# Kernel tuning notes

Measured on AMD Instinct MI355X. Metric: run time of the kernel, lower is better.

## Reference

```python
import jax, jax.numpy as jnp
import numpy as np

DIM = 256; HEADS = 8; DK = 64; DV = 64; FH = 32; FW = 32; B = 16
INK = HEADS * DK; INV = HEADS * DV; N = FH * FW
SCALE = DK ** -0.5; EPS = 1e-5


def _pos_indices():
    pos = np.stack(np.meshgrid(np.arange(FH), np.arange(FW), indexing='ij'), axis=-1).reshape(-1, 2)
    rel = np.abs(pos[:, None, :] - pos[None, :, :])  # [N,N,2]
    return jnp.asarray(rel[..., 0] * FW + rel[..., 1], jnp.int32)  # [N,N]


def _bn(x, g, b, m, v):
    # eval-mode BatchNorm2d over channel axis 1
    s = (g / jnp.sqrt(v + EPS))
    return x * s[None, :, None, None] + (b - m * s)[None, :, None, None]


def setup_inputs() -> dict:
    key = jax.random.key(0)
    ks = jax.random.split(key, 24)
    f32 = jnp.float32
    def bn_params(k, c):
        k1, k2, k3, k4 = jax.random.split(k, 4)
        return (jax.random.normal(k1, (c,), f32) * 0.1 + 1.0,
                jax.random.normal(k2, (c,), f32) * 0.1,
                jax.random.normal(k3, (c,), f32) * 0.1,
                jax.random.uniform(k4, (c,), f32) + 0.5)
    gq, bq, mq, vq = bn_params(ks[1], INK)
    gk, bk, mk, vk = bn_params(ks[3], INK)
    gv, bv, mv, vv = bn_params(ks[5], INV)
    go, bo, mo, vo = bn_params(ks[7], DIM)
    return {
        'x': jax.random.normal(ks[0], (B, DIM, FH, FW), f32),
        'wq': jax.random.normal(ks[2], (INK, DIM), f32) * (DIM ** -0.5),
        'gq': gq, 'bq': bq, 'mq': mq, 'vq': vq,
        'wk': jax.random.normal(ks[4], (INK, DIM), f32) * (DIM ** -0.5),
        'gk': gk, 'bk': bk, 'mk': mk, 'vk': vk,
        'wv': jax.random.normal(ks[6], (INV, DIM), f32) * (DIM ** -0.5),
        'gv': gv, 'bv': bv, 'mv': mv, 'vv': vv,
        'emb': jax.random.normal(ks[8], (N, HEADS), f32) * 0.02,
        'w_out': jax.random.normal(ks[9], (DIM, INV), f32) * (INV ** -0.5),
        'b_out': jax.random.normal(ks[10], (DIM,), f32) * 0.02,
        'go': go, 'bo': bo, 'mo': mo, 'vo': vo,
        'pos_indices': _pos_indices(),
    }


def reference(x, wq, gq, bq, mq, vq, wk, gk, bk, mk, vk, wv, gv, bv, mv, vv,
              emb, w_out, b_out, go, bo, mo, vo, pos_indices):
    b = x.shape[0]
    # 1x1 conv == channel matmul
    q = _bn(jnp.einsum('bchw,oc->bohw', x, wq), gq, bq, mq, vq)
    k = _bn(jnp.einsum('bchw,oc->bohw', x, wk), gk, bk, mk, vk)
    v = _bn(jnp.einsum('bchw,oc->bohw', x, wv), gv, bv, mv, vv)
    # 'b (h d) x y -> b h (x y) d'
    def split_heads(t, d):
        return t.reshape(b, HEADS, d, N).transpose(0, 1, 3, 2)
    q = split_heads(q, DK); k = split_heads(k, DK); v = split_heads(v, DV)
    dots = jnp.einsum('bhid,bhjd->bhij', q, k) * SCALE  # [b,h,N,N]
    bias = emb[pos_indices]                               # [N,N,h] gather
    dots = dots + jnp.transpose(bias, (2, 0, 1))[None] / SCALE
    attn = jax.nn.softmax(dots, axis=-1)
    out = jnp.einsum('bhij,bhjd->bhid', attn, v)
    out = out.transpose(0, 1, 3, 2).reshape(b, INV, FH, FW)  # 'b h (x y) d -> b (h d) x y'
    hs = out * jnp.clip(out + 3.0, 0.0, 6.0) / 6.0           # Hardswish
    y = jnp.einsum('bchw,oc->bohw', hs, w_out) + b_out[None, :, None, None]
    return _bn(y, go, bo, mo, vo)
```

## Files before the change

kernel.cpp:

```cpp
#include <hip/hip_runtime.h>

typedef __attribute__((ext_vector_type(4))) float f32x4;
typedef __attribute__((ext_vector_type(8))) _Float16 f16x8;
typedef __attribute__((ext_vector_type(4))) _Float16 f16x4;

static __device__ __forceinline__ f32x4 mfma16f(f16x8 a, f16x8 b, f32x4 c) {
    return __builtin_amdgcn_mfma_f32_16x16x32_f16(a, b, c, 0, 0, 0);
}

__global__ __launch_bounds__(256) void prep(
    const float* __restrict__ x,
    const float* __restrict__ s0, const float* __restrict__ s1,
    const float* __restrict__ s2, const float* __restrict__ s3,
    _Float16* __restrict__ d0h, _Float16* __restrict__ d0l,
    _Float16* __restrict__ d1h, _Float16* __restrict__ d1l,
    _Float16* __restrict__ d2h, _Float16* __restrict__ d2l,
    _Float16* __restrict__ d3h, _Float16* __restrict__ d3l,
    _Float16* __restrict__ xth, _Float16* __restrict__ xtl)
{
    __shared__ float lt[32][36];
    const int t = threadIdx.x;
    const int bid = blockIdx.x;
    if (bid < 2048) {
        const int seg = bid >> 9;
        const int i = (bid & 511) * 256 + t;
        const float* src = (seg == 0) ? s0 : (seg == 1) ? s1 : (seg == 2) ? s2 : s3;
        _Float16* dh = (seg == 0) ? d0h : (seg == 1) ? d1h : (seg == 2) ? d2h : d3h;
        _Float16* dl = (seg == 0) ? d0l : (seg == 1) ? d1l : (seg == 2) ? d2l : d3l;
        const float f = src[i];
        const _Float16 h = (_Float16)f;
        dh[i] = h;
        dl[i] = (_Float16)(f - (float)h);
    } else {
        const int bid2 = bid - 2048;
        const int c0 = (bid2 & 7) * 32, hw0 = ((bid2 >> 3) & 31) * 32, b = bid2 >> 8;
        {
            const int cl = t >> 3, hw4 = (t & 7) * 4;
            *(f32x4*)&lt[cl][hw4] = *(const f32x4*)&x[((size_t)(b * 256 + c0 + cl)) * 1024 + hw0 + hw4];
        }
        __syncthreads();
        {
            const int hwl = t >> 3, c4 = (t & 7) * 4;
            f16x4 hv, lv;
#pragma unroll
            for (int e = 0; e < 4; ++e) {
                const float f = lt[c4 + e][hwl];
                const _Float16 h = (_Float16)f;
                hv[e] = h;
                lv[e] = (_Float16)(f - (float)h);
            }
            const size_t off = ((size_t)(b * 1024 + hw0 + hwl)) * 256 + c0 + c4;
            *(f16x4*)(xth + off) = hv;
            *(f16x4*)(xtl + off) = lv;
        }
    }
}

__global__ __launch_bounds__(256, 4) void qkv_mfma(
    const _Float16* __restrict__ xth, const _Float16* __restrict__ xtl,
    const _Float16* __restrict__ wqh, const _Float16* __restrict__ wql,
    const _Float16* __restrict__ wkh, const _Float16* __restrict__ wkl,
    const _Float16* __restrict__ wvh, const _Float16* __restrict__ wvl,
    const float* __restrict__ gq, const float* __restrict__ bq, const float* __restrict__ mq, const float* __restrict__ vq,
    const float* __restrict__ gk, const float* __restrict__ bk, const float* __restrict__ mk, const float* __restrict__ vk,
    const float* __restrict__ gv, const float* __restrict__ bv, const float* __restrict__ mv, const float* __restrict__ vv,
    _Float16* __restrict__ qh, _Float16* __restrict__ ql,
    _Float16* __restrict__ kh,
    _Float16* __restrict__ vt)
{
    __shared__ _Float16 Ah[128][64];
    __shared__ _Float16 Al[128][64];
    __shared__ float sc_l[64], tc_l[64];

    const int t = threadIdx.x;
    const int bn = blockIdx.x;
    const int m0 = blockIdx.y * 128;
    const int proj = bn >> 3;
    const int o0 = (bn & 7) * 64;
    const int bimg = m0 >> 10;
    const int nb = m0 & 1023;

    const _Float16* Wh = (proj == 0) ? wqh : (proj == 1) ? wkh : wvh;
    const _Float16* Wl = (proj == 0) ? wql : (proj == 1) ? wkl : wvl;
    const float* G  = (proj == 0) ? gq : (proj == 1) ? gk : gv;
    const float* Bt = (proj == 0) ? bq : (proj == 1) ? bk : bv;
    const float* Mn = (proj == 0) ? mq : (proj == 1) ? mk : mv;
    const float* Vr = (proj == 0) ? vq : (proj == 1) ? vk : vv;

    if (t < 64) {
        const int o = o0 + t;
        float s = G[o] / sqrtf(Vr[o] + 1e-5f);
        float tt = Bt[o] - Mn[o] * s;
        if (proj == 0) { s *= 0.125f; tt *= 0.125f; }
        sc_l[t] = s; tc_l[t] = tt;
    }

    const int wave = t >> 6, lane = t & 63;
    const int quad = lane >> 4, l16 = lane & 15;
    const int wm = (wave >> 1) * 64;
    const int wn = (wave & 1) * 32;

    const int srow = wave * 32;
    const int lr8 = lane >> 3;
    const int lsl = lane & 7;

    f32x4 acc[8] = {};

    for (int c0 = 0; c0 < 256; c0 += 64) {
#pragma unroll
        for (int p = 0; p < 4; ++p) {
            const int r = srow + p * 8 + lr8;
            const int sg = lsl ^ (r & 7);
            const size_t goff = ((size_t)(bimg * 1024 + nb + r)) * 256 + c0 + sg * 8;
            __builtin_amdgcn_global_load_lds(
                (const __attribute__((address_space(1))) void*)(xth + goff),
                (__attribute__((address_space(3))) void*)&Ah[srow + p * 8][0], 16, 0, 0);
            __builtin_amdgcn_global_load_lds(
                (const __attribute__((address_space(1))) void*)(xtl + goff),
                (__attribute__((address_space(3))) void*)&Al[srow + p * 8][0], 16, 0, 0);
        }
        __syncthreads();

#pragma unroll
        for (int kk = 0; kk < 2; ++kk) {
            f16x8 ah[4], al[4], bh[2], bl[2];
#pragma unroll
            for (int nj = 0; nj < 2; ++nj) {
                const size_t off = ((size_t)(o0 + wn + nj * 16 + l16)) * 256 + c0 + kk * 32 + quad * 8;
                bh[nj] = *(const f16x8*)(Wh + off);
                if (proj < 2) bl[nj] = *(const f16x8*)(Wl + off);
            }
#pragma unroll
            for (int mi = 0; mi < 4; ++mi) {
                const int arow = wm + mi * 16 + l16;
                const int sl = ((kk * 4 + quad) ^ (arow & 7)) * 8;
                ah[mi] = *(const f16x8*)&Ah[arow][sl];
                al[mi] = *(const f16x8*)&Al[arow][sl];
            }
            if (proj < 2) {
#pragma unroll
                for (int nj = 0; nj < 2; ++nj)
#pragma unroll
                    for (int mi = 0; mi < 4; ++mi) {
                        f32x4 a = acc[nj * 4 + mi];
                        a = mfma16f(bh[nj], ah[mi], a);
                        a = mfma16f(bh[nj], al[mi], a);
                        a = mfma16f(bl[nj], ah[mi], a);
                        acc[nj * 4 + mi] = a;
                    }
            } else {
#pragma unroll
                for (int mi = 0; mi < 4; ++mi)
#pragma unroll
                    for (int nj = 0; nj < 2; ++nj) {
                        f32x4 a = acc[mi * 2 + nj];
                        a = mfma16f(ah[mi], bh[nj], a);
                        a = mfma16f(al[mi], bh[nj], a);
                        acc[mi * 2 + nj] = a;
                    }
            }
        }
        __syncthreads();
    }

    if (proj < 2) {
        _Float16* Oh = (proj == 0) ? qh : kh;
#pragma unroll
        for (int nj = 0; nj < 2; ++nj) {
            const int olb = wn + nj * 16 + quad * 4;
            const int ob = o0 + olb;
            const int head = ob >> 6, d0 = ob & 63;
#pragma unroll
            for (int mi = 0; mi < 4; ++mi) {
                const int n = nb + wm + mi * 16 + l16;
                f16x4 hv, lv;
#pragma unroll
                for (int rr = 0; rr < 4; ++rr) {
                    const float val = acc[nj * 4 + mi][rr] * sc_l[olb + rr] + tc_l[olb + rr];
                    const _Float16 h = (_Float16)val;
                    hv[rr] = h;
                    lv[rr] = (_Float16)(val - (float)h);
                }
                const size_t off = (((size_t)(bimg * 8 + head)) * 1024 + n) * 64 + d0;
                *(f16x4*)(Oh + off) = hv;
                if (proj == 0) *(f16x4*)(ql + off) = lv;
            }
        }
    } else {
#pragma unroll
        for (int nj = 0; nj < 2; ++nj) {
            const int olb = wn + nj * 16 + l16;
            const int o = o0 + olb;
            const int head = o >> 6, d = o & 63;
            const float s = sc_l[olb], tt = tc_l[olb];
#pragma unroll
            for (int mi = 0; mi < 4; ++mi) {
                const int n0 = nb + wm + mi * 16 + quad * 4;
                f16x4 v4;
#pragma unroll
                for (int rr = 0; rr < 4; ++rr) v4[rr] = (_Float16)(acc[mi * 2 + nj][rr] * s + tt);
                *(f16x4*)(vt + (((size_t)(bimg * 8 + head)) * 64 + d) * 1024 + n0) = v4;
            }
        }
    }
}

__global__ __launch_bounds__(512, 4) void attn_mfma(
    const _Float16* __restrict__ qh, const _Float16* __restrict__ ql,
    const _Float16* __restrict__ kh,
    const _Float16* __restrict__ vt,
    const float* __restrict__ emb,
    _Float16* __restrict__ hsh)
{
    __shared__ float    emb_s[1024];
    __shared__ _Float16 kth[64][76];
    __shared__ _Float16 vts[64][76];

    const int t = threadIdx.x;
    const int bid = blockIdx.x;
    const int bh = bid & 127, qb = bid >> 7;
    const int b = bh >> 3, h = bh & 7;
    const int wave = t >> 6, lane = t & 63;
    const int quad = lane >> 4, l16 = lane & 15;
    const int q0 = qb * 128 + wave * 16;
    const float L2E = 1.44269504f;

    for (int i = t; i < 1024; i += 512) emb_s[i] = (8.0f * emb[i * 8 + h] - 12.0f) * L2E;

    const size_t base = (size_t)bh * 65536;

    f16x8 qfh[2], qfl[2];
#pragma unroll
    for (int kk = 0; kk < 2; ++kk) {
        const size_t off = base + (size_t)(q0 + l16) * 64 + kk * 32 + quad * 8;
        qfh[kk] = *(const f16x8*)(qh + off);
        qfl[kk] = *(const f16x8*)(ql + off);
    }

    const int ig0 = q0 + l16;
    const int xi = ig0 >> 5, yi = ig0 & 31;

    const int sr = t >> 3;
    const int scs = (t & 7) * 8;

    f16x8 pkh, pvv;
    pkh = *(const f16x8*)(kh + base + (size_t)sr * 64 + scs);
    pvv = *(const f16x8*)(vt + base + (size_t)sr * 1024 + scs);

    f32x4 ao[4] = {};
    float lsum = 0.0f;

    for (int jb = 0; jb < 16; ++jb) {
        __syncthreads();
        *(f16x8*)&kth[sr][scs] = pkh;
        *(f16x8*)&vts[sr][scs] = pvv;
        __syncthreads();
        if (jb < 15) {
            pkh = *(const f16x8*)(kh + base + (size_t)((jb + 1) * 64 + sr) * 64 + scs);
            pvv = *(const f16x8*)(vt + base + (size_t)sr * 1024 + (jb + 1) * 64 + scs);
        }

#pragma unroll
        for (int nj = 0; nj < 4; ++nj) {
            const f16x8 kf0 = *(const f16x8*)&kth[nj * 16 + l16][quad * 8];
            const f16x8 kf1 = *(const f16x8*)&kth[nj * 16 + l16][32 + quad * 8];

            f32x4 ss = {};
            __builtin_amdgcn_s_setprio(1);
            ss = mfma16f(kf0, qfh[0], ss);
            ss = mfma16f(kf0, qfl[0], ss);
            ss = mfma16f(kf1, qfh[1], ss);
            ss = mfma16f(kf1, qfl[1], ss);
            __builtin_amdgcn_s_setprio(0);

            const int xj = 2 * jb + (nj >> 1);
            const int yj0 = ((nj & 1) << 4) + quad * 4;
            const int dxo = abs(xi - xj) << 5;
            const int yq = yi - yj0;
            const float p0 = __builtin_amdgcn_exp2f(fmaf(ss[0], L2E, emb_s[dxo + abs(yq)]));
            const float p1 = __builtin_amdgcn_exp2f(fmaf(ss[1], L2E, emb_s[dxo + abs(yq - 1)]));
            const float p2 = __builtin_amdgcn_exp2f(fmaf(ss[2], L2E, emb_s[dxo + abs(yq - 2)]));
            const float p3 = __builtin_amdgcn_exp2f(fmaf(ss[3], L2E, emb_s[dxo + abs(yq - 3)]));
            lsum += (p0 + p1) + (p2 + p3);
            f16x4 pa;
            pa[0] = (_Float16)p0; pa[1] = (_Float16)p1;
            pa[2] = (_Float16)p2; pa[3] = (_Float16)p3;

            f16x4 vf[4];
#pragma unroll
            for (int dj = 0; dj < 4; ++dj)
                vf[dj] = *(const f16x4*)&vts[dj * 16 + l16][nj * 16 + quad * 4];
            __builtin_amdgcn_s_setprio(1);
#pragma unroll
            for (int dj = 0; dj < 4; ++dj)
                ao[dj] = __builtin_amdgcn_mfma_f32_16x16x16f16(pa, vf[dj], ao[dj], 0, 0, 0);
            __builtin_amdgcn_s_setprio(0);
        }
    }

    float l = lsum;
    l += __shfl_xor(l, 16, 64);
    l += __shfl_xor(l, 32, 64);
    float inv[4];
#pragma unroll
    for (int r = 0; r < 4; ++r)
        inv[r] = 1.0f / __shfl(l, quad * 4 + r, 64);
#pragma unroll
    for (int r = 0; r < 4; ++r) {
        const int ig = q0 + quad * 4 + r;
#pragma unroll
        for (int dj = 0; dj < 4; ++dj) {
            const float o = ao[dj][r] * inv[r];
            const float hsw = o * fminf(fmaxf(o + 3.0f, 0.0f), 6.0f) * (1.0f / 6.0f);
            hsh[((size_t)(b * 1024 + ig)) * 512 + h * 64 + dj * 16 + l16] = (_Float16)hsw;
        }
    }
}

__global__ __launch_bounds__(256) void out_mfma(
    const _Float16* __restrict__ hsh,
    const _Float16* __restrict__ woh, const _Float16* __restrict__ wol,
    const float* __restrict__ b_out, const float* __restrict__ go, const float* __restrict__ bo,
    const float* __restrict__ mo, const float* __restrict__ vo, float* __restrict__ y)
{
    __shared__ _Float16 Ah[64][136];

    const int t = threadIdx.x;
    const int m0 = blockIdx.x * 64;
    const int o0 = blockIdx.y * 128;
    const int bimg = m0 >> 10, nb = m0 & 1023;
    const int wave = t >> 6, lane = t & 63;
    const int quad = lane >> 4, l16 = lane & 15;
    const int wm = (wave >> 1) * 32, wn = (wave & 1) * 64;

    f32x4 acc[2][4] = {};
    f16x8 bh[4], bl[4], nbh[4], nbl[4];

#pragma unroll
    for (int nj = 0; nj < 4; ++nj) {
        const size_t off = ((size_t)(o0 + wn + nj * 16 + l16)) * 512 + quad * 8;
        bh[nj] = *(const f16x8*)(woh + off);
        bl[nj] = *(const f16x8*)(wol + off);
    }

#pragma unroll
    for (int it = 0; it < 16; ++it) {
        const int c0 = (it >> 2) * 128, kk = it & 3;
        if (kk == 0) {
            __syncthreads();
            const int cs = (t & 7) * 16;
#pragma unroll
            for (int p = 0; p < 2; ++p) {
                const int r = (t >> 3) + p * 32;
                *(f16x8*)&Ah[r][cs]     = *(const f16x8*)(hsh + ((size_t)(m0 + r)) * 512 + c0 + cs);
                *(f16x8*)&Ah[r][cs + 8] = *(const f16x8*)(hsh + ((size_t)(m0 + r)) * 512 + c0 + cs + 8);
            }
            __syncthreads();
        }
        if (it < 15) {
            const int nit = it + 1;
            const int nc0 = (nit >> 2) * 128, nkk = nit & 3;
#pragma unroll
            for (int nj = 0; nj < 4; ++nj) {
                const size_t off = ((size_t)(o0 + wn + nj * 16 + l16)) * 512 + nc0 + nkk * 32 + quad * 8;
                nbh[nj] = *(const f16x8*)(woh + off);
                nbl[nj] = *(const f16x8*)(wol + off);
            }
        }
        f16x8 ah[2];
#pragma unroll
        for (int mi = 0; mi < 2; ++mi)
            ah[mi] = *(const f16x8*)&Ah[wm + mi * 16 + l16][kk * 32 + quad * 8];
#pragma unroll
        for (int mi = 0; mi < 2; ++mi)
#pragma unroll
            for (int nj = 0; nj < 4; ++nj) {
                acc[mi][nj] = mfma16f(ah[mi], bh[nj], acc[mi][nj]);
                acc[mi][nj] = mfma16f(ah[mi], bl[nj], acc[mi][nj]);
            }
#pragma unroll
        for (int nj = 0; nj < 4; ++nj) { bh[nj] = nbh[nj]; bl[nj] = nbl[nj]; }
    }

#pragma unroll
    for (int nj = 0; nj < 4; ++nj) {
        const int o = o0 + wn + nj * 16 + l16;
        const float s = go[o] / sqrtf(vo[o] + 1e-5f);
        const float tt = bo[o] - mo[o] * s;
        const float bf = b_out[o];
#pragma unroll
        for (int mi = 0; mi < 2; ++mi) {
            const int hw = nb + wm + mi * 16 + quad * 4;
            f32x4 v4;
#pragma unroll
            for (int rr = 0; rr < 4; ++rr) v4[rr] = (acc[mi][nj][rr] + bf) * s + tt;
            *(f32x4*)&y[((size_t)(bimg * 256 + o)) * 1024 + hw] = v4;
        }
    }
}

extern "C" void kernel_launch(void* const* d_in, const int* in_sizes, int n_in,
                              void* d_out, int out_size, void* d_ws, size_t ws_size,
                              hipStream_t stream) {
    const float* x     = (const float*)d_in[0];
    const float* wq    = (const float*)d_in[1];
    const float* gq    = (const float*)d_in[2];
    const float* bq    = (const float*)d_in[3];
    const float* mq    = (const float*)d_in[4];
    const float* vq    = (const float*)d_in[5];
    const float* wk    = (const float*)d_in[6];
    const float* gk    = (const float*)d_in[7];
    const float* bk    = (const float*)d_in[8];
    const float* mk    = (const float*)d_in[9];
    const float* vk    = (const float*)d_in[10];
    const float* wv    = (const float*)d_in[11];
    const float* gv    = (const float*)d_in[12];
    const float* bv    = (const float*)d_in[13];
    const float* mv    = (const float*)d_in[14];
    const float* vv    = (const float*)d_in[15];
    const float* emb   = (const float*)d_in[16];
    const float* w_out = (const float*)d_in[17];
    const float* b_out = (const float*)d_in[18];
    const float* go    = (const float*)d_in[19];
    const float* bo    = (const float*)d_in[20];
    const float* mo    = (const float*)d_in[21];
    const float* vo    = (const float*)d_in[22];

    _Float16* us = (_Float16*)d_ws;
    _Float16* xth = us;
    _Float16* xtl = us + 4194304;
    _Float16* hsh = us;
    _Float16* wsp = us + 16777216;
    _Float16* wqh = wsp,            *wql = wsp + 131072;
    _Float16* wkh = wsp + 262144,   *wkl = wsp + 393216;
    _Float16* wvh = wsp + 524288,   *wvl = wsp + 655360;
    _Float16* woh = wsp + 786432,   *wol = wsp + 917504;
    _Float16* qv  = us + 17825792;
    _Float16* qhw = qv,             *qlw = qv + 8388608;
    _Float16* khw = qv + 16777216;
    _Float16* vtw = qv + 33554432;

    prep<<<6144, 256, 0, stream>>>(x, wq, wk, wv, w_out,
                                   wqh, wql, wkh, wkl, wvh, wvl, woh, wol,
                                   xth, xtl);

    qkv_mfma<<<dim3(24, 128), 256, 0, stream>>>(
        xth, xtl, wqh, wql, wkh, wkl, wvh, wvl,
        gq, bq, mq, vq, gk, bk, mk, vk, gv, bv, mv, vv,
        qhw, qlw, khw, vtw);

    attn_mfma<<<1024, 512, 0, stream>>>(
        qhw, qlw, khw, vtw, emb, hsh);

    out_mfma<<<dim3(256, 2), 256, 0, stream>>>(
        hsh, woh, wol, b_out, go, bo, mo, vo, (float*)d_out);
}
```

Measured before the change: 327.8 us.

## Widen QKV projection tile to 128 outputs and register-prefetch next K slice

The QKV projection kernel now runs 512-thread blocks that each compute 128 output channels instead of 64, halving the grid and halving how often each activation tile is reloaded. The async global-to-LDS loads with XOR swizzle are replaced by register prefetch of the next 64-channel slice, overlapped with the MFMA work on the current slice, and LDS rows are padded to 72 elements in place of the swizzle. The aim is more reuse of the staged x tile and overlap of global loads with compute. In exchange, register pressure rises and the padded layout may still cause some LDS bank conflicts.

```diff
diff --git a/kernel.cpp b/kernel.cpp
--- a/kernel.cpp
+++ b/kernel.cpp
@@ -56,7 +56,7 @@
     }
 }
 
-__global__ __launch_bounds__(256, 4) void qkv_mfma(
+__global__ __launch_bounds__(512, 4) void qkv_mfma(
     const _Float16* __restrict__ xth, const _Float16* __restrict__ xtl,
     const _Float16* __restrict__ wqh, const _Float16* __restrict__ wql,
     const _Float16* __restrict__ wkh, const _Float16* __restrict__ wkl,
@@ -68,15 +68,15 @@
     _Float16* __restrict__ kh,
     _Float16* __restrict__ vt)
 {
-    __shared__ _Float16 Ah[128][64];
-    __shared__ _Float16 Al[128][64];
-    __shared__ float sc_l[64], tc_l[64];
+    __shared__ _Float16 Ah[128][72];
+    __shared__ _Float16 Al[128][72];
+    __shared__ float sc_l[128], tc_l[128];
 
     const int t = threadIdx.x;
     const int bn = blockIdx.x;
     const int m0 = blockIdx.y * 128;
-    const int proj = bn >> 3;
-    const int o0 = (bn & 7) * 64;
+    const int proj = bn >> 2;
+    const int o0 = (bn & 3) * 128;
     const int bimg = m0 >> 10;
     const int nb = m0 & 1023;
 
@@ -87,7 +87,7 @@
     const float* Mn = (proj == 0) ? mq : (proj == 1) ? mk : mv;
     const float* Vr = (proj == 0) ? vq : (proj == 1) ? vk : vv;
 
-    if (t < 64) {
+    if (t < 128) {
         const int o = o0 + t;
         float s = G[o] / sqrtf(Vr[o] + 1e-5f);
         float tt = Bt[o] - Mn[o] * s;
@@ -97,30 +97,38 @@
 
     const int wave = t >> 6, lane = t & 63;
     const int quad = lane >> 4, l16 = lane & 15;
-    const int wm = (wave >> 1) * 64;
-    const int wn = (wave & 1) * 32;
-
-    const int srow = wave * 32;
-    const int lr8 = lane >> 3;
-    const int lsl = lane & 7;
+    const int wm = (wave >> 2) * 64;
+    const int wn = (wave & 3) * 32;
+
+    const int sr = t >> 3;
+    const int scs = (t & 7) * 8;
+
+    f16x8 pxh[2], pxl[2];
+#pragma unroll
+    for (int p = 0; p < 2; ++p) {
+        const size_t off = ((size_t)(bimg * 1024 + nb + sr + p * 64)) * 256 + scs;
+        pxh[p] = *(const f16x8*)(xth + off);
+        pxl[p] = *(const f16x8*)(xtl + off);
+    }
 
     f32x4 acc[8] = {};
 
     for (int c0 = 0; c0 < 256; c0 += 64) {
-#pragma unroll
-        for (int p = 0; p < 4; ++p) {
-            const int r = srow + p * 8 + lr8;
-            const int sg = lsl ^ (r & 7);
-            const size_t goff = ((size_t)(bimg * 1024 + nb + r)) * 256 + c0 + sg * 8;
-            __builtin_amdgcn_global_load_lds(
-                (const __attribute__((address_space(1))) void*)(xth + goff),
-                (__attribute__((address_space(3))) void*)&Ah[srow + p * 8][0], 16, 0, 0);
-            __builtin_amdgcn_global_load_lds(
-                (const __attribute__((address_space(1))) void*)(xtl + goff),
-                (__attribute__((address_space(3))) void*)&Al[srow + p * 8][0], 16, 0, 0);
-        }
         __syncthreads();
-
+#pragma unroll
+        for (int p = 0; p < 2; ++p) {
+            *(f16x8*)&Ah[sr + p * 64][scs] = pxh[p];
+            *(f16x8*)&Al[sr + p * 64][scs] = pxl[p];
+        }
+        __syncthreads();
+        if (c0 < 192) {
+#pragma unroll
+            for (int p = 0; p < 2; ++p) {
+                const size_t off = ((size_t)(bimg * 1024 + nb + sr + p * 64)) * 256 + c0 + 64 + scs;
+                pxh[p] = *(const f16x8*)(xth + off);
+                pxl[p] = *(const f16x8*)(xtl + off);
+            }
+        }
 #pragma unroll
         for (int kk = 0; kk < 2; ++kk) {
             f16x8 ah[4], al[4], bh[2], bl[2];
@@ -132,10 +140,8 @@
             }
 #pragma unroll
             for (int mi = 0; mi < 4; ++mi) {
-                const int arow = wm + mi * 16 + l16;
-                const int sl = ((kk * 4 + quad) ^ (arow & 7)) * 8;
-                ah[mi] = *(const f16x8*)&Ah[arow][sl];
-                al[mi] = *(const f16x8*)&Al[arow][sl];
+                ah[mi] = *(const f16x8*)&Ah[wm + mi * 16 + l16][kk * 32 + quad * 8];
+                al[mi] = *(const f16x8*)&Al[wm + mi * 16 + l16][kk * 32 + quad * 8];
             }
             if (proj < 2) {
 #pragma unroll
@@ -160,7 +166,6 @@
                     }
             }
         }
-        __syncthreads();
     }
 
     if (proj < 2) {
@@ -444,7 +449,7 @@
                                    wqh, wql, wkh, wkl, wvh, wvl, woh, wol,
                                    xth, xtl);
 
-    qkv_mfma<<<dim3(24, 128), 256, 0, stream>>>(
+    qkv_mfma<<<dim3(12, 128), 512, 0, stream>>>(
         xth, xtl, wqh, wql, wkh, wkl, wvh, wvl,
         gq, bq, mq, vq, gk, bk, mk, vk, gv, bv, mv, vv,
         qhw, qlw, khw, vtw);
```

After: 320.2 us. 1.02x faster.
